# Kernel optimization log

Measured on AMD Instinct MI355X. Metric: run time of the kernel, lower is better.

The kernel has to match this reference:

```python
import jax, jax.numpy as jnp
import numpy as np

B, T, E, V, H = 4096, 80, 100, 10000, 64


def setup_inputs() -> dict:
    key = jax.random.key(0)
    ks = jax.random.split(key, 8)
    s = lambda k, sh: (jax.random.normal(k, sh, jnp.float32) * 0.05)
    return {
        "inputs": jax.random.randint(ks[0], (B, T), 0, V),
        "emb": s(ks[1], (V, E)),
        "Wx0": s(ks[2], (E, H)),
        "Wh0": s(ks[3], (H, H)),
        "b0": jnp.zeros((H,), jnp.float32),
        "Wx1": s(ks[4], (H, H)),
        "Wh1": s(ks[5], (H, H)),
        "b1": jnp.zeros((H,), jnp.float32),
        "Wf": s(ks[6], (H, 1)),
        "bf": jnp.zeros((1,), jnp.float32),
    }


def reference(inputs, emb, Wx0, Wh0, b0, Wx1, Wh1, b1, Wf, bf):
    # Embedding lookup: [B, T] int -> [B, T, E]
    x = emb[inputs]
    xT = jnp.swapaxes(x, 0, 1)  # [T, B, E] for scan over time

    def step(carry, xt):
        h0, h1 = carry
        # SimpleRNNCell layer 0: tanh(x@Wx + h@Wh + b)
        h0 = jnp.tanh(xt @ Wx0 + h0 @ Wh0 + b0)
        # SimpleRNNCell layer 1 consumes layer-0 output
        h1 = jnp.tanh(h0 @ Wx1 + h1 @ Wh1 + b1)
        return (h0, h1), None

    init = (jnp.zeros((B, H), x.dtype), jnp.zeros((B, H), x.dtype))
    (h0_last, h1_last), _ = jax.lax.scan(step, init, xT)
    # Dense(1) + sigmoid on last timestep's layer-1 hidden state
    return jax.nn.sigmoid(h1_last @ Wf + bf)  # [B, 1]
```

## Files before the change

kernel.cpp:

```cpp
#include <hip/hip_runtime.h>
#include <stdint.h>

#define BB 4096
#define TT 80
#define EE 100
#define VV 10000
#define HH 64

typedef float f32x4 __attribute__((ext_vector_type(4)));
typedef _Float16 f16x8 __attribute__((ext_vector_type(8)));

union AF { uint32_t u[4]; f16x8 v; _Float16 e[8]; };
union PU { uint32_t u[8]; f16x8 f[2]; _Float16 e[16]; };

__device__ __forceinline__ uint32_t pk_f16(float lo, float hi){
  uint32_t r;
  asm("v_cvt_pkrtz_f16_f32 %0, %1, %2" : "=v"(r) : "v"(lo), "v"(hi));
  return r;
}
__device__ __forceinline__ uint32_t pk_add(uint32_t a, uint32_t b){
  uint32_t r;
  asm("v_pk_add_f16 %0, %1, %2" : "=v"(r) : "v"(a), "v"(b));
  return r;
}
__device__ __forceinline__ uint32_t tanh_pk(uint32_t x, uint32_t one, uint32_t c3){
  uint32_t r, x2;
  asm("v_pk_mul_f16 %0, %1, %1" : "=v"(x2) : "v"(x));
  asm("v_pk_fma_f16 %0, %1, %2, %3" : "=v"(x2) : "v"(x2), "v"(c3), "v"(one));
  asm("v_pk_mul_f16 %0, %1, %2" : "=v"(r) : "v"(x), "v"(x2));
  return r;
}
__device__ __forceinline__ void tick_barrier(){
  asm volatile("s_waitcnt lgkmcnt(0)" ::: "memory");
  __builtin_amdgcn_s_barrier();
  asm volatile("" ::: "memory");
}

#define MF(Af, Bf, Cf) __builtin_amdgcn_mfma_f32_16x16x32_f16((Af).v, (Bf), (Cf), 0, 0, 0)
#define I4C(v, s) ((s)==0?(v).x:(s)==1?(v).y:(s)==2?(v).z:(v).w)

__global__ __launch_bounds__(64) void build_table_mfma(
    const float* __restrict__ emb, const float* __restrict__ Wx0,
    const float* __restrict__ b0, float* __restrict__ table){
  const int lane = threadIdx.x & 63;
  const int c = lane & 15, g = lane >> 4;
  const int v0 = blockIdx.x * 16;

  AF Aem[4];
  const float* er = emb + (v0 + c)*EE;
  #pragma unroll
  for (int kk = 0; kk < 4; kk++){
    #pragma unroll
    for (int p = 0; p < 4; p++){
      int k0 = 32*kk + 8*g + 2*p;
      int ks0 = (k0   < EE) ? k0   : 0;
      int ks1 = (k0+1 < EE) ? k0+1 : 0;
      float e0 = er[ks0]; if (k0   >= EE) e0 = 0.f;
      float e1 = er[ks1]; if (k0+1 >= EE) e1 = 0.f;
      Aem[kk].u[p] = pk_f16(e0, e1);
    }
  }
  AF Bw[4][4];
  #pragma unroll
  for (int qp = 0; qp < 4; qp++){
    #pragma unroll
    for (int kk = 0; kk < 4; kk++){
      #pragma unroll
      for (int p = 0; p < 4; p++){
        int k0 = 32*kk + 8*g + 2*p;
        int ks0 = (k0   < EE) ? k0   : 0;
        int ks1 = (k0+1 < EE) ? k0+1 : 0;
        float w0v = Wx0[ks0*HH + 16*qp + c]; if (k0   >= EE) w0v = 0.f;
        float w1v = Wx0[ks1*HH + 16*qp + c]; if (k0+1 >= EE) w1v = 0.f;
        Bw[qp][kk].u[p] = pk_f16(w0v, w1v);
      }
    }
  }
  f32x4 acc[4];
  #pragma unroll
  for (int qp = 0; qp < 4; qp++){
    float bv = b0[16*qp + c];
    acc[qp].x = bv; acc[qp].y = bv; acc[qp].z = bv; acc[qp].w = bv;
  }
  #pragma unroll
  for (int kk = 0; kk < 4; kk++)
    #pragma unroll
    for (int qp = 0; qp < 4; qp++)
      acc[qp] = __builtin_amdgcn_mfma_f32_16x16x32_f16(Aem[kk].v, Bw[qp][kk].v, acc[qp], 0, 0, 0);
  #pragma unroll
  for (int qp = 0; qp < 4; qp++)
    #pragma unroll
    for (int i = 0; i < 4; i++)
      table[(v0 + 4*g + i)*HH + 16*qp + c] = acc[qp][i];
}

__global__ __launch_bounds__(192, 1) void rnn_fused6(
    const int* __restrict__ inputs, const float* __restrict__ table,
    const float* __restrict__ Wh0, const float* __restrict__ Wx1,
    const float* __restrict__ Wh1, const float* __restrict__ b1,
    const float* __restrict__ Wf, const float* __restrict__ bfp,
    float* __restrict__ out)
{
  __shared__ uint2 LB[8192];
  uint2* Hh = LB;
  uint2* Pc = LB + 4096;

  const int tid = threadIdx.x;
  const int wid = tid >> 6;
  const int lane = tid & 63;
  const int c = lane & 15, g = lane >> 4;
  const int b0r = blockIdx.x * 16;
  const uint32_t one = 0x3C003C00u, c3 = 0xB555B555u;

  if (wid == 0){
    AF A0[4][2];
    #pragma unroll
    for (int q = 0; q < 4; q++)
      #pragma unroll
      for (int kk = 0; kk < 2; kk++)
        #pragma unroll
        for (int p = 0; p < 4; p++){
          int hid = 32*kk + 16*(p>>1) + 4*g + 2*(p&1);
          int o0 = hid*HH + 16*q + c;
          A0[q][kk].u[p] = pk_f16(Wh0[o0], Wh0[o0+HH]);
        }
    PU P0;
    #pragma unroll
    for (int i = 0; i < 8; i++) P0.u[i] = 0u;

    const char* tb = (const char*)table;
    const char* ib = (const char*)inputs;
    const uint32_t gb = (uint32_t)(g << 4);
    const uint32_t ibase = (uint32_t)((b0r + c) * TT * 4);

    f32x4 z[4][4];
    int4 idxHi;
    {
      int4 iA = *(const int4*)(ib + ibase);
      idxHi   = *(const int4*)(ib + ibase + 16);
      #pragma unroll
      for (int s = 0; s < 4; s++){
        uint32_t vo = ((uint32_t)I4C(iA, s) << 8) | gb;
        #pragma unroll
        for (int q = 0; q < 4; q++) z[s][q] = *(const f32x4*)(tb + vo + 64*q);
      }
    }

    #pragma unroll 1
    for (int it = 0; it < 12; ++it){
      if (it < 10){
        int toff = 8*it + 8; if (toff > 72) toff = 72;
        int4 nA = *(const int4*)(ib + ibase + (uint32_t)(toff*4));
        int4 nB = *(const int4*)(ib + ibase + (uint32_t)(toff*4) + 16);
        uint2* H = Hh + (it & 1)*2048;
        #pragma unroll
        for (int s = 0; s < 8; ++s){
          const int zs = s & 3;
          int idxv = (s < 4) ? I4C(idxHi, s) : I4C(nA, s-4);
          f32x4 a0 = MF(A0[0][0], P0.f[0], z[zs][0]);
          f32x4 a1 = MF(A0[1][0], P0.f[0], z[zs][1]);
          f32x4 a2 = MF(A0[2][0], P0.f[0], z[zs][2]);
          f32x4 a3 = MF(A0[3][0], P0.f[0], z[zs][3]);
          { uint32_t vo = ((uint32_t)idxv << 8) | gb;
            z[zs][0] = *(const f32x4*)(tb + vo);
            z[zs][1] = *(const f32x4*)(tb + vo + 64);
            z[zs][2] = *(const f32x4*)(tb + vo + 128);
            z[zs][3] = *(const f32x4*)(tb + vo + 192); }
          a0 = MF(A0[0][1], P0.f[1], a0);
          a1 = MF(A0[1][1], P0.f[1], a1);
          a2 = MF(A0[2][1], P0.f[1], a2);
          a3 = MF(A0[3][1], P0.f[1], a3);
          P0.u[0] = tanh_pk(pk_f16(a0.x, a0.y), one, c3);
          P0.u[1] = tanh_pk(pk_f16(a0.z, a0.w), one, c3);
          P0.u[2] = tanh_pk(pk_f16(a1.x, a1.y), one, c3);
          P0.u[3] = tanh_pk(pk_f16(a1.z, a1.w), one, c3);
          P0.u[4] = tanh_pk(pk_f16(a2.x, a2.y), one, c3);
          P0.u[5] = tanh_pk(pk_f16(a2.z, a2.w), one, c3);
          P0.u[6] = tanh_pk(pk_f16(a3.x, a3.y), one, c3);
          P0.u[7] = tanh_pk(pk_f16(a3.z, a3.w), one, c3);
          H[(s*4 + 0)*64 + lane] = make_uint2(P0.u[0], P0.u[1]);
          H[(s*4 + 1)*64 + lane] = make_uint2(P0.u[2], P0.u[3]);
          H[(s*4 + 2)*64 + lane] = make_uint2(P0.u[4], P0.u[5]);
          H[(s*4 + 3)*64 + lane] = make_uint2(P0.u[6], P0.u[7]);
        }
        idxHi = nB;
      }
      tick_barrier();
    }
  } else if (wid == 1){
    AF A1[4][2];
    #pragma unroll
    for (int q = 0; q < 4; q++)
      #pragma unroll
      for (int kk = 0; kk < 2; kk++)
        #pragma unroll
        for (int p = 0; p < 4; p++){
          int hid = 32*kk + 16*(p>>1) + 4*g + 2*(p&1);
          int o0 = hid*HH + 16*q + c;
          A1[q][kk].u[p] = pk_f16(Wx1[o0], Wx1[o0+HH]);
        }
    f32x4 b1c[4];
    #pragma unroll
    for (int q = 0; q < 4; q++) b1c[q] = *(const f32x4*)(b1 + 16*q + 4*g);

    #pragma unroll 1
    for (int it = 0; it < 12; ++it){
      if (it >= 1 && it <= 10){
        const int sl = (it - 1) & 1;
        uint2* H  = Hh + sl*2048;
        uint2* PW = Pc + sl*2048;
        #pragma unroll
        for (int s = 0; s < 8; ++s){
          uint2 r0 = H[(s*4 + 0)*64 + lane];
          uint2 r1 = H[(s*4 + 1)*64 + lane];
          uint2 r2 = H[(s*4 + 2)*64 + lane];
          uint2 r3 = H[(s*4 + 3)*64 + lane];
          PU h;
          h.u[0]=r0.x; h.u[1]=r0.y; h.u[2]=r1.x; h.u[3]=r1.y;
          h.u[4]=r2.x; h.u[5]=r2.y; h.u[6]=r3.x; h.u[7]=r3.y;
          f32x4 d0 = MF(A1[0][0], h.f[0], b1c[0]);
          f32x4 d1 = MF(A1[1][0], h.f[0], b1c[1]);
          f32x4 d2 = MF(A1[2][0], h.f[0], b1c[2]);
          f32x4 d3 = MF(A1[3][0], h.f[0], b1c[3]);
          d0 = MF(A1[0][1], h.f[1], d0);
          d1 = MF(A1[1][1], h.f[1], d1);
          d2 = MF(A1[2][1], h.f[1], d2);
          d3 = MF(A1[3][1], h.f[1], d3);
          PW[(s*4 + 0)*64 + lane] = make_uint2(pk_f16(d0.x, d0.y), pk_f16(d0.z, d0.w));
          PW[(s*4 + 1)*64 + lane] = make_uint2(pk_f16(d1.x, d1.y), pk_f16(d1.z, d1.w));
          PW[(s*4 + 2)*64 + lane] = make_uint2(pk_f16(d2.x, d2.y), pk_f16(d2.z, d2.w));
          PW[(s*4 + 3)*64 + lane] = make_uint2(pk_f16(d3.x, d3.y), pk_f16(d3.z, d3.w));
        }
      }
      tick_barrier();
    }
  } else {
    AF A2[4][2];
    #pragma unroll
    for (int q = 0; q < 4; q++)
      #pragma unroll
      for (int kk = 0; kk < 2; kk++)
        #pragma unroll
        for (int p = 0; p < 4; p++){
          int hid = 32*kk + 16*(p>>1) + 4*g + 2*(p&1);
          int o0 = hid*HH + 16*q + c;
          A2[q][kk].u[p] = pk_f16(Wh1[o0], Wh1[o0+HH]);
        }
    PU P1;
    #pragma unroll
    for (int i = 0; i < 8; i++) P1.u[i] = 0u;
    const f32x4 kz = {0.f, 0.f, 0.f, 0.f};

    #pragma unroll 1
    for (int it = 0; it < 12; ++it){
      if (it >= 2){
        const int sl = (it - 2) & 1;
        uint2* PR = Pc + sl*2048;
        #pragma unroll
        for (int s = 0; s < 8; ++s){
          uint2 q0 = PR[(s*4 + 0)*64 + lane];
          uint2 q1 = PR[(s*4 + 1)*64 + lane];
          uint2 q2 = PR[(s*4 + 2)*64 + lane];
          uint2 q3 = PR[(s*4 + 3)*64 + lane];
          f32x4 e0 = MF(A2[0][0], P1.f[0], kz);
          f32x4 e1 = MF(A2[1][0], P1.f[0], kz);
          f32x4 e2 = MF(A2[2][0], P1.f[0], kz);
          f32x4 e3 = MF(A2[3][0], P1.f[0], kz);
          e0 = MF(A2[0][1], P1.f[1], e0);
          e1 = MF(A2[1][1], P1.f[1], e1);
          e2 = MF(A2[2][1], P1.f[1], e2);
          e3 = MF(A2[3][1], P1.f[1], e3);
          P1.u[0] = tanh_pk(pk_add(pk_f16(e0.x, e0.y), q0.x), one, c3);
          P1.u[1] = tanh_pk(pk_add(pk_f16(e0.z, e0.w), q0.y), one, c3);
          P1.u[2] = tanh_pk(pk_add(pk_f16(e1.x, e1.y), q1.x), one, c3);
          P1.u[3] = tanh_pk(pk_add(pk_f16(e1.z, e1.w), q1.y), one, c3);
          P1.u[4] = tanh_pk(pk_add(pk_f16(e2.x, e2.y), q2.x), one, c3);
          P1.u[5] = tanh_pk(pk_add(pk_f16(e2.z, e2.w), q2.y), one, c3);
          P1.u[6] = tanh_pk(pk_add(pk_f16(e3.x, e3.y), q3.x), one, c3);
          P1.u[7] = tanh_pk(pk_add(pk_f16(e3.z, e3.w), q3.y), one, c3);
        }
      }
      tick_barrier();
    }

    float sv = 0.f;
    #pragma unroll
    for (int q = 0; q < 4; q++)
      #pragma unroll
      for (int p = 0; p < 2; p++){
        AF u; u.u[0] = P1.u[2*q + p];
        int hb = 16*q + 4*g + 2*p;
        sv = fmaf((float)u.e[0], Wf[hb],   sv);
        sv = fmaf((float)u.e[1], Wf[hb+1], sv);
      }
    sv += __shfl_xor(sv, 16, 64);
    sv += __shfl_xor(sv, 32, 64);
    sv += bfp[0];
    float r = 1.0f / (1.0f + __expf(-sv));
    if (lane < 16) out[b0r + lane] = r;
  }
}

extern "C" void kernel_launch(void* const* d_in, const int* in_sizes, int n_in,
                              void* d_out, int out_size, void* d_ws, size_t ws_size,
                              hipStream_t stream){
  const int*   inputs = (const int*)d_in[0];
  const float* emb = (const float*)d_in[1];
  const float* Wx0 = (const float*)d_in[2];
  const float* Wh0 = (const float*)d_in[3];
  const float* b0  = (const float*)d_in[4];
  const float* Wx1 = (const float*)d_in[5];
  const float* Wh1 = (const float*)d_in[6];
  const float* b1  = (const float*)d_in[7];
  const float* Wf  = (const float*)d_in[8];
  const float* bf  = (const float*)d_in[9];
  float* out   = (float*)d_out;
  float* table = (float*)d_ws;

  build_table_mfma<<<dim3(VV/16), dim3(64), 0, stream>>>(emb, Wx0, b0, table);
  rnn_fused6<<<dim3(BB/16), dim3(192), 0, stream>>>(inputs, table, Wh0, Wx1, Wh1, b1, Wf, bf, out);
}
```

Before: 33.54 us.

## Process two independent 16-row batch tiles per block to interleave recurrences

Each block now handles 32 batch rows as two independent 16-row chains (U and V), with each warp alternating steps between the two chains. Interleaving two independent dependency chains lets MFMA and tanh latency of one chain be hidden behind the other, within the same LDS buffers and barriers. The grid halves to 128 blocks, which leaves fewer blocks than the 256 CUs on the device and raises register pressure per wave.

After: 46.78 us. +39.5%, slower.

```diff
diff --git a/kernel.cpp b/kernel.cpp
--- a/kernel.cpp
+++ b/kernel.cpp
@@ -37,7 +37,6 @@
 }
 
 #define MF(Af, Bf, Cf) __builtin_amdgcn_mfma_f32_16x16x32_f16((Af).v, (Bf), (Cf), 0, 0, 0)
-#define I4C(v, s) ((s)==0?(v).x:(s)==1?(v).y:(s)==2?(v).z:(v).w)
 
 __global__ __launch_bounds__(64) void build_table_mfma(
     const float* __restrict__ emb, const float* __restrict__ Wx0,
@@ -94,7 +93,80 @@
       table[(v0 + 4*g + i)*HH + 16*qp + c] = acc[qp][i];
 }
 
-__global__ __launch_bounds__(192, 1) void rnn_fused6(
+#define W0STEP(PX, ZX, ZI, IDXV, HP) { \
+  f32x4 a0 = MF(A0[0][0], PX.f[0], ZX[ZI][0]); \
+  f32x4 a1 = MF(A0[1][0], PX.f[0], ZX[ZI][1]); \
+  f32x4 a2 = MF(A0[2][0], PX.f[0], ZX[ZI][2]); \
+  f32x4 a3 = MF(A0[3][0], PX.f[0], ZX[ZI][3]); \
+  { uint32_t vo = ((uint32_t)(IDXV) << 8) | gb; \
+    ZX[ZI][0] = *(const f32x4*)(tb + vo); \
+    ZX[ZI][1] = *(const f32x4*)(tb + vo + 64); \
+    ZX[ZI][2] = *(const f32x4*)(tb + vo + 128); \
+    ZX[ZI][3] = *(const f32x4*)(tb + vo + 192); } \
+  a0 = MF(A0[0][1], PX.f[1], a0); \
+  a1 = MF(A0[1][1], PX.f[1], a1); \
+  a2 = MF(A0[2][1], PX.f[1], a2); \
+  a3 = MF(A0[3][1], PX.f[1], a3); \
+  PX.u[0] = tanh_pk(pk_f16(a0.x, a0.y), one, c3); \
+  PX.u[1] = tanh_pk(pk_f16(a0.z, a0.w), one, c3); \
+  PX.u[2] = tanh_pk(pk_f16(a1.x, a1.y), one, c3); \
+  PX.u[3] = tanh_pk(pk_f16(a1.z, a1.w), one, c3); \
+  PX.u[4] = tanh_pk(pk_f16(a2.x, a2.y), one, c3); \
+  PX.u[5] = tanh_pk(pk_f16(a2.z, a2.w), one, c3); \
+  PX.u[6] = tanh_pk(pk_f16(a3.x, a3.y), one, c3); \
+  PX.u[7] = tanh_pk(pk_f16(a3.z, a3.w), one, c3); \
+  (HP)[0*64 + lane] = make_uint2(PX.u[0], PX.u[1]); \
+  (HP)[1*64 + lane] = make_uint2(PX.u[2], PX.u[3]); \
+  (HP)[2*64 + lane] = make_uint2(PX.u[4], PX.u[5]); \
+  (HP)[3*64 + lane] = make_uint2(PX.u[6], PX.u[7]); \
+}
+
+#define W1STEP(HP, PP) { \
+  uint2 r0 = (HP)[0*64 + lane]; \
+  uint2 r1 = (HP)[1*64 + lane]; \
+  uint2 r2 = (HP)[2*64 + lane]; \
+  uint2 r3 = (HP)[3*64 + lane]; \
+  PU h; \
+  h.u[0]=r0.x; h.u[1]=r0.y; h.u[2]=r1.x; h.u[3]=r1.y; \
+  h.u[4]=r2.x; h.u[5]=r2.y; h.u[6]=r3.x; h.u[7]=r3.y; \
+  f32x4 d0 = MF(A1[0][0], h.f[0], b1c[0]); \
+  f32x4 d1 = MF(A1[1][0], h.f[0], b1c[1]); \
+  f32x4 d2 = MF(A1[2][0], h.f[0], b1c[2]); \
+  f32x4 d3 = MF(A1[3][0], h.f[0], b1c[3]); \
+  d0 = MF(A1[0][1], h.f[1], d0); \
+  d1 = MF(A1[1][1], h.f[1], d1); \
+  d2 = MF(A1[2][1], h.f[1], d2); \
+  d3 = MF(A1[3][1], h.f[1], d3); \
+  (PP)[0*64 + lane] = make_uint2(pk_f16(d0.x, d0.y), pk_f16(d0.z, d0.w)); \
+  (PP)[1*64 + lane] = make_uint2(pk_f16(d1.x, d1.y), pk_f16(d1.z, d1.w)); \
+  (PP)[2*64 + lane] = make_uint2(pk_f16(d2.x, d2.y), pk_f16(d2.z, d2.w)); \
+  (PP)[3*64 + lane] = make_uint2(pk_f16(d3.x, d3.y), pk_f16(d3.z, d3.w)); \
+}
+
+#define W2STEP(PX, PP) { \
+  uint2 q0 = (PP)[0*64 + lane]; \
+  uint2 q1 = (PP)[1*64 + lane]; \
+  uint2 q2 = (PP)[2*64 + lane]; \
+  uint2 q3 = (PP)[3*64 + lane]; \
+  f32x4 e0 = MF(A2[0][0], PX.f[0], kz); \
+  f32x4 e1 = MF(A2[1][0], PX.f[0], kz); \
+  f32x4 e2 = MF(A2[2][0], PX.f[0], kz); \
+  f32x4 e3 = MF(A2[3][0], PX.f[0], kz); \
+  e0 = MF(A2[0][1], PX.f[1], e0); \
+  e1 = MF(A2[1][1], PX.f[1], e1); \
+  e2 = MF(A2[2][1], PX.f[1], e2); \
+  e3 = MF(A2[3][1], PX.f[1], e3); \
+  PX.u[0] = tanh_pk(pk_add(pk_f16(e0.x, e0.y), q0.x), one, c3); \
+  PX.u[1] = tanh_pk(pk_add(pk_f16(e0.z, e0.w), q0.y), one, c3); \
+  PX.u[2] = tanh_pk(pk_add(pk_f16(e1.x, e1.y), q1.x), one, c3); \
+  PX.u[3] = tanh_pk(pk_add(pk_f16(e1.z, e1.w), q1.y), one, c3); \
+  PX.u[4] = tanh_pk(pk_add(pk_f16(e2.x, e2.y), q2.x), one, c3); \
+  PX.u[5] = tanh_pk(pk_add(pk_f16(e2.z, e2.w), q2.y), one, c3); \
+  PX.u[6] = tanh_pk(pk_add(pk_f16(e3.x, e3.y), q3.x), one, c3); \
+  PX.u[7] = tanh_pk(pk_add(pk_f16(e3.z, e3.w), q3.y), one, c3); \
+}
+
+__global__ __launch_bounds__(192, 1) void rnn_fused7(
     const int* __restrict__ inputs, const float* __restrict__ table,
     const float* __restrict__ Wh0, const float* __restrict__ Wx1,
     const float* __restrict__ Wh1, const float* __restrict__ b1,
@@ -102,14 +174,11 @@
     float* __restrict__ out)
 {
   __shared__ uint2 LB[8192];
-  uint2* Hh = LB;
-  uint2* Pc = LB + 4096;
-
   const int tid = threadIdx.x;
   const int wid = tid >> 6;
   const int lane = tid & 63;
   const int c = lane & 15, g = lane >> 4;
-  const int b0r = blockIdx.x * 16;
+  const int b0r = blockIdx.x * 32;
   const uint32_t one = 0x3C003C00u, c3 = 0xB555B555u;
 
   if (wid == 0){
@@ -124,66 +193,48 @@
           int o0 = hid*HH + 16*q + c;
           A0[q][kk].u[p] = pk_f16(Wh0[o0], Wh0[o0+HH]);
         }
-    PU P0;
-    #pragma unroll
-    for (int i = 0; i < 8; i++) P0.u[i] = 0u;
+    PU P0U, P0V;
+    #pragma unroll
+    for (int i = 0; i < 8; i++){ P0U.u[i] = 0u; P0V.u[i] = 0u; }
 
     const char* tb = (const char*)table;
     const char* ib = (const char*)inputs;
     const uint32_t gb = (uint32_t)(g << 4);
-    const uint32_t ibase = (uint32_t)((b0r + c) * TT * 4);
-
-    f32x4 z[4][4];
-    int4 idxHi;
+    const uint32_t ibU = (uint32_t)((b0r +      c) * TT * 4);
+    const uint32_t ibV = (uint32_t)((b0r + 16 + c) * TT * 4);
+
+    int4 WU = *(const int4*)(ib + ibU);
+    int4 WV = *(const int4*)(ib + ibV);
+    f32x4 zU[2][4], zV[2][4];
     {
-      int4 iA = *(const int4*)(ib + ibase);
-      idxHi   = *(const int4*)(ib + ibase + 16);
-      #pragma unroll
-      for (int s = 0; s < 4; s++){
-        uint32_t vo = ((uint32_t)I4C(iA, s) << 8) | gb;
-        #pragma unroll
-        for (int q = 0; q < 4; q++) z[s][q] = *(const f32x4*)(tb + vo + 64*q);
+      uint32_t u0 = ((uint32_t)WU.x << 8) | gb, u1 = ((uint32_t)WU.y << 8) | gb;
+      uint32_t v0 = ((uint32_t)WV.x << 8) | gb, v1 = ((uint32_t)WV.y << 8) | gb;
+      #pragma unroll
+      for (int q = 0; q < 4; q++){
+        zU[0][q] = *(const f32x4*)(tb + u0 + 64*q);
+        zU[1][q] = *(const f32x4*)(tb + u1 + 64*q);
+        zV[0][q] = *(const f32x4*)(tb + v0 + 64*q);
+        zV[1][q] = *(const f32x4*)(tb + v1 + 64*q);
       }
     }
 
     #pragma unroll 1
-    for (int it = 0; it < 12; ++it){
-      if (it < 10){
-        int toff = 8*it + 8; if (toff > 72) toff = 72;
-        int4 nA = *(const int4*)(ib + ibase + (uint32_t)(toff*4));
-        int4 nB = *(const int4*)(ib + ibase + (uint32_t)(toff*4) + 16);
-        uint2* H = Hh + (it & 1)*2048;
-        #pragma unroll
-        for (int s = 0; s < 8; ++s){
-          const int zs = s & 3;
-          int idxv = (s < 4) ? I4C(idxHi, s) : I4C(nA, s-4);
-          f32x4 a0 = MF(A0[0][0], P0.f[0], z[zs][0]);
-          f32x4 a1 = MF(A0[1][0], P0.f[0], z[zs][1]);
-          f32x4 a2 = MF(A0[2][0], P0.f[0], z[zs][2]);
-          f32x4 a3 = MF(A0[3][0], P0.f[0], z[zs][3]);
-          { uint32_t vo = ((uint32_t)idxv << 8) | gb;
-            z[zs][0] = *(const f32x4*)(tb + vo);
-            z[zs][1] = *(const f32x4*)(tb + vo + 64);
-            z[zs][2] = *(const f32x4*)(tb + vo + 128);
-            z[zs][3] = *(const f32x4*)(tb + vo + 192); }
-          a0 = MF(A0[0][1], P0.f[1], a0);
-          a1 = MF(A0[1][1], P0.f[1], a1);
-          a2 = MF(A0[2][1], P0.f[1], a2);
-          a3 = MF(A0[3][1], P0.f[1], a3);
-          P0.u[0] = tanh_pk(pk_f16(a0.x, a0.y), one, c3);
-          P0.u[1] = tanh_pk(pk_f16(a0.z, a0.w), one, c3);
-          P0.u[2] = tanh_pk(pk_f16(a1.x, a1.y), one, c3);
-          P0.u[3] = tanh_pk(pk_f16(a1.z, a1.w), one, c3);
-          P0.u[4] = tanh_pk(pk_f16(a2.x, a2.y), one, c3);
-          P0.u[5] = tanh_pk(pk_f16(a2.z, a2.w), one, c3);
-          P0.u[6] = tanh_pk(pk_f16(a3.x, a3.y), one, c3);
-          P0.u[7] = tanh_pk(pk_f16(a3.z, a3.w), one, c3);
-          H[(s*4 + 0)*64 + lane] = make_uint2(P0.u[0], P0.u[1]);
-          H[(s*4 + 1)*64 + lane] = make_uint2(P0.u[2], P0.u[3]);
-          H[(s*4 + 2)*64 + lane] = make_uint2(P0.u[4], P0.u[5]);
-          H[(s*4 + 3)*64 + lane] = make_uint2(P0.u[6], P0.u[7]);
-        }
-        idxHi = nB;
+    for (int it = 0; it < 22; ++it){
+      if (it < 20){
+        int toffN = 4*it + 4; if (toffN > TT - 4) toffN = TT - 4;
+        int4 NU = *(const int4*)(ib + ibU + (uint32_t)(toffN*4));
+        int4 NV = *(const int4*)(ib + ibV + (uint32_t)(toffN*4));
+        uint2* HU = LB + (it & 1)*2048;
+        uint2* HV = HU + 1024;
+        W0STEP(P0U, zU, 0, WU.z, HU + 0*256)
+        W0STEP(P0V, zV, 0, WV.z, HV + 0*256)
+        W0STEP(P0U, zU, 1, WU.w, HU + 1*256)
+        W0STEP(P0V, zV, 1, WV.w, HV + 1*256)
+        W0STEP(P0U, zU, 0, NU.x, HU + 2*256)
+        W0STEP(P0V, zV, 0, NV.x, HV + 2*256)
+        W0STEP(P0U, zU, 1, NU.y, HU + 3*256)
+        W0STEP(P0V, zV, 1, NV.y, HV + 3*256)
+        WU = NU; WV = NV;
       }
       tick_barrier();
     }
@@ -204,32 +255,17 @@
     for (int q = 0; q < 4; q++) b1c[q] = *(const f32x4*)(b1 + 16*q + 4*g);
 
     #pragma unroll 1
-    for (int it = 0; it < 12; ++it){
-      if (it >= 1 && it <= 10){
+    for (int it = 0; it < 22; ++it){
+      if (it >= 1 && it <= 20){
         const int sl = (it - 1) & 1;
-        uint2* H  = Hh + sl*2048;
-        uint2* PW = Pc + sl*2048;
-        #pragma unroll
-        for (int s = 0; s < 8; ++s){
-          uint2 r0 = H[(s*4 + 0)*64 + lane];
-          uint2 r1 = H[(s*4 + 1)*64 + lane];
-          uint2 r2 = H[(s*4 + 2)*64 + lane];
-          uint2 r3 = H[(s*4 + 3)*64 + lane];
-          PU h;
-          h.u[0]=r0.x; h.u[1]=r0.y; h.u[2]=r1.x; h.u[3]=r1.y;
-          h.u[4]=r2.x; h.u[5]=r2.y; h.u[6]=r3.x; h.u[7]=r3.y;
-          f32x4 d0 = MF(A1[0][0], h.f[0], b1c[0]);
-          f32x4 d1 = MF(A1[1][0], h.f[0], b1c[1]);
-          f32x4 d2 = MF(A1[2][0], h.f[0], b1c[2]);
-          f32x4 d3 = MF(A1[3][0], h.f[0], b1c[3]);
-          d0 = MF(A1[0][1], h.f[1], d0);
-          d1 = MF(A1[1][1], h.f[1], d1);
-          d2 = MF(A1[2][1], h.f[1], d2);
-          d3 = MF(A1[3][1], h.f[1], d3);
-          PW[(s*4 + 0)*64 + lane] = make_uint2(pk_f16(d0.x, d0.y), pk_f16(d0.z, d0.w));
-          PW[(s*4 + 1)*64 + lane] = make_uint2(pk_f16(d1.x, d1.y), pk_f16(d1.z, d1.w));
-          PW[(s*4 + 2)*64 + lane] = make_uint2(pk_f16(d2.x, d2.y), pk_f16(d2.z, d2.w));
-          PW[(s*4 + 3)*64 + lane] = make_uint2(pk_f16(d3.x, d3.y), pk_f16(d3.z, d3.w));
+        uint2* HU = LB + sl*2048;
+        uint2* HV = HU + 1024;
+        uint2* PU_ = LB + 4096 + sl*2048;
+        uint2* PV_ = PU_ + 1024;
+        #pragma unroll
+        for (int s = 0; s < 4; ++s){
+          W1STEP(HU + s*256, PU_ + s*256)
+          W1STEP(HV + s*256, PV_ + s*256)
         }
       }
       tick_barrier();
@@ -246,58 +282,51 @@
           int o0 = hid*HH + 16*q + c;
           A2[q][kk].u[p] = pk_f16(Wh1[o0], Wh1[o0+HH]);
         }
-    PU P1;
-    #pragma unroll
-    for (int i = 0; i < 8; i++) P1.u[i] = 0u;
+    PU P1U, P1V;
+    #pragma unroll
+    for (int i = 0; i < 8; i++){ P1U.u[i] = 0u; P1V.u[i] = 0u; }
     const f32x4 kz = {0.f, 0.f, 0.f, 0.f};
 
     #pragma unroll 1
-    for (int it = 0; it < 12; ++it){
+    for (int it = 0; it < 22; ++it){
       if (it >= 2){
         const int sl = (it - 2) & 1;
-        uint2* PR = Pc + sl*2048;
-        #pragma unroll
-        for (int s = 0; s < 8; ++s){
-          uint2 q0 = PR[(s*4 + 0)*64 + lane];
-          uint2 q1 = PR[(s*4 + 1)*64 + lane];
-          uint2 q2 = PR[(s*4 + 2)*64 + lane];
-          uint2 q3 = PR[(s*4 + 3)*64 + lane];
-          f32x4 e0 = MF(A2[0][0], P1.f[0], kz);
-          f32x4 e1 = MF(A2[1][0], P1.f[0], kz);
-          f32x4 e2 = MF(A2[2][0], P1.f[0], kz);
-          f32x4 e3 = MF(A2[3][0], P1.f[0], kz);
-          e0 = MF(A2[0][1], P1.f[1], e0);
-          e1 = MF(A2[1][1], P1.f[1], e1);
-          e2 = MF(A2[2][1], P1.f[1], e2);
-          e3 = MF(A2[3][1], P1.f[1], e3);
-          P1.u[0] = tanh_pk(pk_add(pk_f16(e0.x, e0.y), q0.x), one, c3);
-          P1.u[1] = tanh_pk(pk_add(pk_f16(e0.z, e0.w), q0.y), one, c3);
-          P1.u[2] = tanh_pk(pk_add(pk_f16(e1.x, e1.y), q1.x), one, c3);
-          P1.u[3] = tanh_pk(pk_add(pk_f16(e1.z, e1.w), q1.y), one, c3);
-          P1.u[4] = tanh_pk(pk_add(pk_f16(e2.x, e2.y), q2.x), one, c3);
-          P1.u[5] = tanh_pk(pk_add(pk_f16(e2.z, e2.w), q2.y), one, c3);
-          P1.u[6] = tanh_pk(pk_add(pk_f16(e3.x, e3.y), q3.x), one, c3);
-          P1.u[7] = tanh_pk(pk_add(pk_f16(e3.z, e3.w), q3.y), one, c3);
+        uint2* PU_ = LB + 4096 + sl*2048;
+        uint2* PV_ = PU_ + 1024;
+        #pragma unroll
+        for (int s = 0; s < 4; ++s){
+          W2STEP(P1U, PU_ + s*256)
+          W2STEP(P1V, PV_ + s*256)
         }
       }
       tick_barrier();
     }
 
-    float sv = 0.f;
+    float svU = 0.f, svV = 0.f;
     #pragma unroll
     for (int q = 0; q < 4; q++)
       #pragma unroll
       for (int p = 0; p < 2; p++){
-        AF u; u.u[0] = P1.u[2*q + p];
+        AF uU; uU.u[0] = P1U.u[2*q + p];
+        AF uV; uV.u[0] = P1V.u[2*q + p];
         int hb = 16*q + 4*g + 2*p;
-        sv = fmaf((float)u.e[0], Wf[hb],   sv);
-        sv = fmaf((float)u.e[1], Wf[hb+1], sv);
-      }
-    sv += __shfl_xor(sv, 16, 64);
-    sv += __shfl_xor(sv, 32, 64);
-    sv += bfp[0];
-    float r = 1.0f / (1.0f + __expf(-sv));
-    if (lane < 16) out[b0r + lane] = r;
+        float w0 = Wf[hb], w1 = Wf[hb+1];
+        svU = fmaf((float)uU.e[0], w0, svU);
+        svU = fmaf((float)uU.e[1], w1, svU);
+        svV = fmaf((float)uV.e[0], w0, svV);
+        svV = fmaf((float)uV.e[1], w1, svV);
+      }
+    svU += __shfl_xor(svU, 16, 64);
+    svU += __shfl_xor(svU, 32, 64);
+    svV += __shfl_xor(svV, 16, 64);
+    svV += __shfl_xor(svV, 32, 64);
+    float bfv = bfp[0];
+    float rU = 1.0f / (1.0f + __expf(-(svU + bfv)));
+    float rV = 1.0f / (1.0f + __expf(-(svV + bfv)));
+    if (lane < 16){
+      out[b0r + lane]      = rU;
+      out[b0r + 16 + lane] = rV;
+    }
   }
 }
 
@@ -318,5 +347,5 @@
   float* table = (float*)d_ws;
 
   build_table_mfma<<<dim3(VV/16), dim3(64), 0, stream>>>(emb, Wx0, b0, table);
-  rnn_fused6<<<dim3(BB/16), dim3(192), 0, stream>>>(inputs, table, Wh0, Wx1, Wh1, b1, Wf, bf, out);
-}
+  rnn_fused7<<<dim3(BB/32), dim3(192), 0, stream>>>(inputs, table, Wh0, Wx1, Wh1, b1, Wf, bf, out);
+}
```
